# Kernel tuning notes

Hardware: AMD Instinct MI355X
Metric: run time of the kernel (lower is better)

The kernel has to match this reference:

```python
import jax, jax.numpy as jnp
import numpy as np

BN_EPS = 1e-5

def _conv3x3(x, w):
    # x: [N,C,H,W], w: [O,I,3,3], stride 1, padding 1, no bias
    return jax.lax.conv_general_dilated(
        x, w, window_strides=(1, 1), padding=((1, 1), (1, 1)),
        dimension_numbers=("NCHW", "OIHW", "NCHW"))

def _batchnorm(x, gamma, beta):
    # training-mode BN: batch statistics over (N,H,W)
    mean = jnp.mean(x, axis=(0, 2, 3), keepdims=True)
    var = jnp.mean(jnp.square(x - mean), axis=(0, 2, 3), keepdims=True)
    inv = jax.lax.rsqrt(var + BN_EPS)
    g = gamma.reshape(1, -1, 1, 1)
    b = beta.reshape(1, -1, 1, 1)
    return (x - mean) * inv * g + b

def setup_inputs() -> dict:
    key = jax.random.key(0)
    ks = jax.random.split(key, 3)
    x = jax.random.normal(ks[0], (32, 64, 128, 128), dtype=jnp.float32)
    # He-style scaled 3x3 conv kernels
    w1 = jax.random.normal(ks[1], (64, 64, 3, 3), dtype=jnp.float32) * (2.0 / (64 * 9)) ** 0.5
    w2 = jax.random.normal(ks[2], (64, 64, 3, 3), dtype=jnp.float32) * (2.0 / (64 * 9)) ** 0.5
    return {
        "x": x, "w1": w1, "w2": w2,
        "bn1_gamma": jnp.ones((64,), jnp.float32),
        "bn1_beta": jnp.zeros((64,), jnp.float32),
        "bn2_gamma": jnp.ones((64,), jnp.float32),
        "bn2_beta": jnp.zeros((64,), jnp.float32),
    }

def reference(x, w1, w2, bn1_gamma, bn1_beta, bn2_gamma, bn2_beta):
    out = _batchnorm(_conv3x3(x, w1), bn1_gamma, bn1_beta)
    out = _conv3x3(out, w2)
    out = out + x  # option 'A', stride=1, planes[2]==planes[0] -> identity shortcut
    return _batchnorm(out, bn2_gamma, bn2_beta)
```

## Files before the change

kernel.cpp:

```cpp
#include <hip/hip_runtime.h>
#include <hip/hip_bf16.h>

#define NB 32
#define CH 64
#define HH 128
#define WW 128
#define HW (HH*WW)
#define CHW (CH*HW)
#define NCHW (NB*CHW)
#define CNT_PER_CH ((float)(NB*HW))
#define ROWS 4

typedef __attribute__((ext_vector_type(8)))  short short8;
typedef __attribute__((ext_vector_type(16))) float f32x16;

__device__ __forceinline__ unsigned short f2bf(float f) {
  unsigned u = __builtin_bit_cast(unsigned, f);
  u += 0x7fffu + ((u >> 16) & 1u);
  return (unsigned short)(u >> 16);
}

__device__ __forceinline__ void gld_lds16(const void* g, void* s) {
  __builtin_amdgcn_global_load_lds(
      (const __attribute__((address_space(1))) unsigned int*)g,
      (__attribute__((address_space(3))) unsigned int*)s, 16, 0, 0);
}

__global__ __launch_bounds__(256) void t1_pack(const float* __restrict__ x,
                                               unsigned short* __restrict__ xb) {
  __shared__ __align__(16) unsigned short tmp[CH * WW];
  const int bid = blockIdx.x;
  const int tid = threadIdx.x;
  const float* src = x + (size_t)(bid >> 7) * CHW + (size_t)(bid & 127) * WW;
  for (int i = tid; i < 2048; i += 256) {
    const int ci = i >> 5, wq = i & 31;
    const float4 v = *(const float4*)(src + (size_t)ci * HW + wq * 4);
    unsigned short* d = &tmp[ci * WW + wq * 4];
    d[0] = f2bf(v.x); d[1] = f2bf(v.y); d[2] = f2bf(v.z); d[3] = f2bf(v.w);
  }
  __syncthreads();
  unsigned short* dst = xb + (size_t)bid * 8192;
  for (int i = tid; i < 1024; i += 256) {
    const int cb = i >> 7, w = i & 127;
    const unsigned short* s = &tmp[cb * 8 * WW + w];
    uint4 o;
    o.x = (unsigned)s[0]      | ((unsigned)s[WW]     << 16);
    o.y = (unsigned)s[2*WW]   | ((unsigned)s[3*WW]   << 16);
    o.z = (unsigned)s[4*WW]   | ((unsigned)s[5*WW]   << 16);
    o.w = (unsigned)s[6*WW]   | ((unsigned)s[7*WW]   << 16);
    *(uint4*)(dst + ((size_t)cb * WW + w) * 8) = o;
  }
}

__global__ __launch_bounds__(256) void pack_w(const float* __restrict__ w,
                                              const float* __restrict__ s1,
                                              const float* __restrict__ b1,
                                              unsigned short* __restrict__ wpk,
                                              float* __restrict__ tabs) {
  const int tid = threadIdx.x;
  for (int idx = tid; idx < 36864; idx += 256) {
    const int f = idx >> 9, l = (idx >> 3) & 63, r = idx & 7;
    const int m = f & 1, kq = (f >> 1) & 3, t = f >> 3;
    const int co = (l & 31) + 32 * m;
    const int ci = kq * 16 + (l >> 5) * 8 + r;
    float v = w[co * 576 + ci * 9 + t];
    if (s1) v *= s1[ci];
    wpk[idx] = f2bf(v);
  }
  if (tabs != nullptr && tid < 64) {
    const int co = tid;
    float tb[9];
    for (int t = 0; t < 9; ++t) {
      float a = 0.f;
      for (int ci = 0; ci < 64; ++ci) a += w[co * 576 + ci * 9 + t] * b1[ci];
      tb[t] = a;
    }
    tabs[0*64+co] = tb[0]+tb[1]+tb[2]+tb[3]+tb[4]+tb[5]+tb[6]+tb[7]+tb[8];
    tabs[1*64+co] = tb[0]+tb[1]+tb[2];
    tabs[2*64+co] = tb[6]+tb[7]+tb[8];
    tabs[3*64+co] = tb[0]+tb[3]+tb[6];
    tabs[4*64+co] = tb[2]+tb[5]+tb[8];
    tabs[5*64+co] = tb[0]; tabs[6*64+co] = tb[2];
    tabs[7*64+co] = tb[6]; tabs[8*64+co] = tb[8];
  }
}

template <bool IS2>
__global__ __launch_bounds__(256, 2)
void conv_mfma(const unsigned short* __restrict__ inb,
               const unsigned short* __restrict__ wpack,
               const float* __restrict__ tabs,
               const float* __restrict__ resid,
               unsigned short* __restrict__ outb,
               float* __restrict__ outf,
               float* __restrict__ psum, float* __restrict__ psq) {
  extern __shared__ __align__(16) unsigned short A[];
  const int tid = threadIdx.x, bid = blockIdx.x;
  const int n = bid >> 5, h0 = (bid & 31) << 2;
  const int wv = tid >> 6, lane = tid & 63;
  const int half = lane >> 5, lp = lane & 31;
  const int m  = wv & 1;
  const int nb = (wv >> 1) << 1;

  auto stage = [&](int ir) {
    const int sl = (ir + 4) & 3;
#pragma unroll
    for (int t = 0; t < 4; ++t) {
      const int id = wv + 4 * t;
      const int cb = id >> 1, wh = id & 1;
      unsigned short* dst = &A[(((sl * 8 + cb) * 130) + 1 + wh * 64) * 8];
      if ((unsigned)ir < 128u) {
        const unsigned short* g = inb + ((((size_t)n * 128 + ir) * 8 + cb) << 10)
                                      + (size_t)(wh * 64 + lane) * 8;
        gld_lds16(g, dst);
      } else {
        *(uint4*)(dst + (size_t)lane * 8) = make_uint4(0, 0, 0, 0);
      }
    }
  };

  if (tid < 64) {
    const int sl = tid >> 4, cb = (tid >> 1) & 7, s = (tid & 1) ? 129 : 0;
    *(uint4*)&A[(((sl * 8 + cb) * 130) + s) * 8] = make_uint4(0, 0, 0, 0);
  }

  short8 wr[36];
#pragma unroll
  for (int i = 0; i < 36; ++i) {
    const int f = ((i >> 2) << 3) + ((i & 3) << 1) + m;
    wr[i] = *(const short8*)(wpack + (size_t)f * 512 + (size_t)lane * 8);
  }

  stage(h0 - 1); stage(h0); stage(h0 + 1);

  for (int k = 0; k < ROWS; ++k) {
    const int r = h0 + k;
    __syncthreads();

    float rv[2][16];
    if (IS2) {
#pragma unroll
      for (int nt = 0; nt < 2; ++nt) {
        const int px = (nb + nt) * 32 + lp;
#pragma unroll
        for (int rr = 0; rr < 16; ++rr) {
          const int co = (rr & 3) + ((rr >> 2) << 3) + 4 * half + 32 * m;
          rv[nt][rr] = resid[(((size_t)n * 64 + co) * 128 + r) * 128 + px];
        }
      }
    }

    if (k < ROWS - 1) stage(r + 2);

    const int sl_m1 = (r + 3) & 3, sl_0 = (r + 4) & 3, sl_p1 = (r + 5) & 3;
    const int slot[3] = {sl_m1, sl_0, sl_p1};
    f32x16 acc0 = {}; f32x16 acc1 = {};
#pragma unroll
    for (int kh = 0; kh < 3; ++kh) {
      const int sb = slot[kh] * 8;
#pragma unroll
      for (int kw = 0; kw < 3; ++kw) {
#pragma unroll
        for (int kq = 0; kq < 4; ++kq) {
          const short8 wf = wr[(kh * 3 + kw) * 4 + kq];
          const int cb = kq * 2 + half;
          const unsigned short* base = &A[((sb + cb) * 130) * 8];
          const short8 b0 = *(const short8*)&base[(nb * 32 + lp + kw) * 8];
          const short8 b1 = *(const short8*)&base[((nb + 1) * 32 + lp + kw) * 8];
          acc0 = __builtin_amdgcn_mfma_f32_32x32x16_bf16(wf, b0, acc0, 0, 0, 0);
          acc1 = __builtin_amdgcn_mfma_f32_32x32x16_bf16(wf, b1, acc1, 0, 0, 0);
        }
      }
    }

    if (!IS2) {
      unsigned short* dst = outb + (((size_t)n * 128 + r) << 13);
#pragma unroll
      for (int nt = 0; nt < 2; ++nt) {
        const f32x16& a = nt ? acc1 : acc0;
        const int px = (nb + nt) * 32 + lp;
#pragma unroll
        for (int rq = 0; rq < 4; ++rq) {
          uint2 pk;
          pk.x = (unsigned)f2bf(a[rq*4+0]) | ((unsigned)f2bf(a[rq*4+1]) << 16);
          pk.y = (unsigned)f2bf(a[rq*4+2]) | ((unsigned)f2bf(a[rq*4+3]) << 16);
          *(uint2*)(dst + (((size_t)(rq + 4*m)) << 10) + (size_t)px * 8 + half * 4) = pk;
        }
      }
    } else {
      const bool bh0 = (r == 0), bh1 = (r == 127);
#pragma unroll
      for (int nt = 0; nt < 2; ++nt) {
        f32x16& a = nt ? acc1 : acc0;
        const int px = (nb + nt) * 32 + lp;
        const bool bw0 = (px == 0), bw1 = (px == 127);
#pragma unroll
        for (int rr = 0; rr < 16; ++rr) {
          const int co = (rr & 3) + ((rr >> 2) << 3) + 4 * half + 32 * m;
          float tb = tabs[co];
          if (bh0) tb -= tabs[64 + co];
          if (bh1) tb -= tabs[128 + co];
          if (bw0) tb -= tabs[192 + co];
          if (bw1) tb -= tabs[256 + co];
          if (bh0 && bw0) tb += tabs[320 + co];
          if (bh0 && bw1) tb += tabs[384 + co];
          if (bh1 && bw0) tb += tabs[448 + co];
          if (bh1 && bw1) tb += tabs[512 + co];
          const float v = a[rr] + tb + rv[nt][rr];
          outf[(((size_t)n * 64 + co) * 128 + r) * 128 + px] = v;
          a[rr] = v;
        }
      }
    }

#pragma unroll
    for (int rr = 0; rr < 16; ++rr) {
      float s = acc0[rr] + acc1[rr];
      float q = acc0[rr] * acc0[rr] + acc1[rr] * acc1[rr];
      s += __shfl_xor(s, 1);  q += __shfl_xor(q, 1);
      s += __shfl_xor(s, 2);  q += __shfl_xor(q, 2);
      s += __shfl_xor(s, 4);  q += __shfl_xor(q, 4);
      s += __shfl_xor(s, 8);  q += __shfl_xor(q, 8);
      s += __shfl_xor(s, 16); q += __shfl_xor(q, 16);
      if (lp == 0) {
        const int co = (rr & 3) + ((rr >> 2) << 3) + 4 * half + 32 * m;
        atomicAdd(&psum[(bid & 63) * 64 + co], s);
        atomicAdd(&psq [(bid & 63) * 64 + co], q);
      }
    }
  }
}

__global__ void finalize_bn(const float* __restrict__ psum, const float* __restrict__ psq,
                            const float* __restrict__ gamma, const float* __restrict__ beta,
                            float* __restrict__ scale, float* __restrict__ bias) {
  const int c = threadIdx.x;
  if (c < 64) {
    float s = 0.f, q = 0.f;
    for (int i = 0; i < 64; ++i) { s += psum[i * 64 + c]; q += psq[i * 64 + c]; }
    const float mean = s * (1.0f / CNT_PER_CH);
    const float var  = q * (1.0f / CNT_PER_CH) - mean * mean;
    const float inv  = rsqrtf(var + 1e-5f);
    const float sc   = inv * gamma[c];
    scale[c] = sc;
    bias[c]  = beta[c] - mean * sc;
  }
}

__global__ __launch_bounds__(256)
void apply_bn_k(float* __restrict__ out,
                const float* __restrict__ scale, const float* __restrict__ bias) {
  __shared__ float sc[CH], bs[CH];
  if (threadIdx.x < CH) { sc[threadIdx.x] = scale[threadIdx.x]; bs[threadIdx.x] = bias[threadIdx.x]; }
  __syncthreads();
  const size_t total4 = NCHW / 4;
  for (size_t i = (size_t)blockIdx.x * blockDim.x + threadIdx.x; i < total4;
       i += (size_t)gridDim.x * blockDim.x) {
    float4 v = reinterpret_cast<float4*>(out)[i];
    const int c = (int)(((i * 4) >> 14) & 63);
    const float s = sc[c], b = bs[c];
    v.x = fmaf(v.x, s, b);
    v.y = fmaf(v.y, s, b);
    v.z = fmaf(v.z, s, b);
    v.w = fmaf(v.w, s, b);
    reinterpret_cast<float4*>(out)[i] = v;
  }
}

extern "C" void kernel_launch(void* const* d_in, const int* in_sizes, int n_in,
                              void* d_out, int out_size, void* d_ws, size_t ws_size,
                              hipStream_t stream) {
  const float* x  = (const float*)d_in[0];
  const float* w1 = (const float*)d_in[1];
  const float* w2 = (const float*)d_in[2];
  const float* g1 = (const float*)d_in[3];
  const float* b1 = (const float*)d_in[4];
  const float* g2 = (const float*)d_in[5];
  const float* b2 = (const float*)d_in[6];
  float* out = (float*)d_out;
  char* ws = (char*)d_ws;

  unsigned short* XB  = (unsigned short*)ws;
  unsigned short* Y1B = (unsigned short*)(ws + 67108864);
  unsigned short* W2P = (unsigned short*)ws;
  float* TABS = (float*)(ws + 73728);
  float* SC1  = (float*)(ws + 76032);
  float* BS1  = (float*)(ws + 76288);
  float* SC2  = (float*)(ws + 76544);
  float* BS2  = (float*)(ws + 76800);
  float* P2S  = (float*)(ws + 77056);
  float* P2Q  = (float*)(ws + 93440);
  char* ob = (char*)d_out;
  unsigned short* W1P = (unsigned short*)ob;
  float* P1S = (float*)(ob + 73728);
  float* P1Q = (float*)(ob + 90112);

  const size_t conv_lds = 4 * 8 * 130 * 8 * sizeof(unsigned short);

  hipMemsetAsync(ob + 73728, 0, 32768, stream);
  pack_w<<<1, 256, 0, stream>>>(w1, nullptr, nullptr, W1P, nullptr);
  t1_pack<<<4096, 256, 0, stream>>>(x, XB);
  conv_mfma<false><<<1024, 256, conv_lds, stream>>>(XB, W1P, nullptr, nullptr,
                                                    Y1B, nullptr, P1S, P1Q);
  finalize_bn<<<1, 64, 0, stream>>>(P1S, P1Q, g1, b1, SC1, BS1);
  hipMemsetAsync(ws + 77056, 0, 32768, stream);
  pack_w<<<1, 256, 0, stream>>>(w2, SC1, BS1, W2P, TABS);
  conv_mfma<true><<<1024, 256, conv_lds, stream>>>(Y1B, W2P, TABS, x,
                                                   nullptr, out, P2S, P2Q);
  finalize_bn<<<1, 64, 0, stream>>>(P2S, P2Q, g2, b2, SC2, BS2);
  apply_bn_k<<<2048, 256, 0, stream>>>(out, SC2, BS2);
}
```

Measured before the change: 559.1 us.

## Replace per-row atomic BN stat reduction with per-block partials, drop memsets

Batch-norm sums and squared sums are now accumulated in registers across all rows of a block. They are reduced through wave shuffles and LDS, and each block writes one plain partial per channel, replacing the atomicAdds issued every row. The finalize kernel now uses 256 threads to reduce 1024 block partials, so both hipMemsetAsync calls are removed. This cuts atomic traffic and launches in exchange for a larger partial buffer and a longer serial reduction in finalize.

Measured after the change: 555.0 us. About the same (-0.7%).

```diff
diff --git a/kernel.cpp b/kernel.cpp
--- a/kernel.cpp
+++ b/kernel.cpp
@@ -10,6 +10,7 @@
 #define NCHW (NB*CHW)
 #define CNT_PER_CH ((float)(NB*HW))
 #define ROWS 4
+#define NBLK 1024
 
 typedef __attribute__((ext_vector_type(8)))  short short8;
 typedef __attribute__((ext_vector_type(16))) float f32x16;
@@ -93,7 +94,7 @@
                const float* __restrict__ resid,
                unsigned short* __restrict__ outb,
                float* __restrict__ outf,
-               float* __restrict__ psum, float* __restrict__ psq) {
+               float* __restrict__ pblk_s, float* __restrict__ pblk_q) {
   extern __shared__ __align__(16) unsigned short A[];
   const int tid = threadIdx.x, bid = blockIdx.x;
   const int n = bid >> 5, h0 = (bid & 31) << 2;
@@ -130,6 +131,10 @@
     const int f = ((i >> 2) << 3) + ((i & 3) << 1) + m;
     wr[i] = *(const short8*)(wpack + (size_t)f * 512 + (size_t)lane * 8);
   }
+
+  float ss[16], qq[16];
+#pragma unroll
+  for (int i = 0; i < 16; ++i) { ss[i] = 0.f; qq[i] = 0.f; }
 
   stage(h0 - 1); stage(h0); stage(h0 + 1);
 
@@ -215,29 +220,54 @@
 
 #pragma unroll
     for (int rr = 0; rr < 16; ++rr) {
-      float s = acc0[rr] + acc1[rr];
-      float q = acc0[rr] * acc0[rr] + acc1[rr] * acc1[rr];
-      s += __shfl_xor(s, 1);  q += __shfl_xor(q, 1);
-      s += __shfl_xor(s, 2);  q += __shfl_xor(q, 2);
-      s += __shfl_xor(s, 4);  q += __shfl_xor(q, 4);
-      s += __shfl_xor(s, 8);  q += __shfl_xor(q, 8);
-      s += __shfl_xor(s, 16); q += __shfl_xor(q, 16);
-      if (lp == 0) {
-        const int co = (rr & 3) + ((rr >> 2) << 3) + 4 * half + 32 * m;
-        atomicAdd(&psum[(bid & 63) * 64 + co], s);
-        atomicAdd(&psq [(bid & 63) * 64 + co], q);
-      }
-    }
-  }
-}
-
-__global__ void finalize_bn(const float* __restrict__ psum, const float* __restrict__ psq,
-                            const float* __restrict__ gamma, const float* __restrict__ beta,
-                            float* __restrict__ scale, float* __restrict__ bias) {
-  const int c = threadIdx.x;
-  if (c < 64) {
-    float s = 0.f, q = 0.f;
-    for (int i = 0; i < 64; ++i) { s += psum[i * 64 + c]; q += psq[i * 64 + c]; }
+      ss[rr] += acc0[rr] + acc1[rr];
+      qq[rr] += acc0[rr] * acc0[rr] + acc1[rr] * acc1[rr];
+    }
+  }
+
+  __syncthreads();
+  float* SLs = (float*)A;
+  float* SLq = SLs + 128;
+  const int p = wv >> 1;
+#pragma unroll
+  for (int rr = 0; rr < 16; ++rr) {
+    float s = ss[rr], q = qq[rr];
+    s += __shfl_xor(s, 1);  q += __shfl_xor(q, 1);
+    s += __shfl_xor(s, 2);  q += __shfl_xor(q, 2);
+    s += __shfl_xor(s, 4);  q += __shfl_xor(q, 4);
+    s += __shfl_xor(s, 8);  q += __shfl_xor(q, 8);
+    s += __shfl_xor(s, 16); q += __shfl_xor(q, 16);
+    if (lp == 0) {
+      const int co = (rr & 3) + ((rr >> 2) << 3) + 4 * half + 32 * m;
+      SLs[p * 64 + co] = s;
+      SLq[p * 64 + co] = q;
+    }
+  }
+  __syncthreads();
+  if (tid < 64) {
+    pblk_s[(size_t)bid * 64 + tid] = SLs[tid] + SLs[64 + tid];
+  } else if (tid < 128) {
+    const int co = tid - 64;
+    pblk_q[(size_t)bid * 64 + co] = SLq[co] + SLq[64 + co];
+  }
+}
+
+__global__ __launch_bounds__(256)
+void finalize_bn(const float* __restrict__ pblk_s, const float* __restrict__ pblk_q,
+                 const float* __restrict__ gamma, const float* __restrict__ beta,
+                 float* __restrict__ scale, float* __restrict__ bias) {
+  __shared__ float ls[4][64], lq[4][64];
+  const int c = threadIdx.x & 63, seg = threadIdx.x >> 6;
+  float s = 0.f, q = 0.f;
+  for (int i = seg * (NBLK / 4); i < (seg + 1) * (NBLK / 4); ++i) {
+    s += pblk_s[(size_t)i * 64 + c];
+    q += pblk_q[(size_t)i * 64 + c];
+  }
+  ls[seg][c] = s; lq[seg][c] = q;
+  __syncthreads();
+  if (threadIdx.x < 64) {
+    s = ls[0][c] + ls[1][c] + ls[2][c] + ls[3][c];
+    q = lq[0][c] + lq[1][c] + lq[2][c] + lq[3][c];
     const float mean = s * (1.0f / CNT_PER_CH);
     const float var  = q * (1.0f / CNT_PER_CH) - mean * mean;
     const float inv  = rsqrtf(var + 1e-5f);
@@ -288,25 +318,23 @@
   float* BS1  = (float*)(ws + 76288);
   float* SC2  = (float*)(ws + 76544);
   float* BS2  = (float*)(ws + 76800);
-  float* P2S  = (float*)(ws + 77056);
-  float* P2Q  = (float*)(ws + 93440);
+  float* P2S  = (float*)(ws + 131072);
+  float* P2Q  = (float*)(ws + 131072 + 262144);
   char* ob = (char*)d_out;
   unsigned short* W1P = (unsigned short*)ob;
   float* P1S = (float*)(ob + 73728);
-  float* P1Q = (float*)(ob + 90112);
+  float* P1Q = (float*)(ob + 73728 + 262144);
 
   const size_t conv_lds = 4 * 8 * 130 * 8 * sizeof(unsigned short);
 
-  hipMemsetAsync(ob + 73728, 0, 32768, stream);
   pack_w<<<1, 256, 0, stream>>>(w1, nullptr, nullptr, W1P, nullptr);
   t1_pack<<<4096, 256, 0, stream>>>(x, XB);
-  conv_mfma<false><<<1024, 256, conv_lds, stream>>>(XB, W1P, nullptr, nullptr,
+  conv_mfma<false><<<NBLK, 256, conv_lds, stream>>>(XB, W1P, nullptr, nullptr,
                                                     Y1B, nullptr, P1S, P1Q);
-  finalize_bn<<<1, 64, 0, stream>>>(P1S, P1Q, g1, b1, SC1, BS1);
-  hipMemsetAsync(ws + 77056, 0, 32768, stream);
+  finalize_bn<<<1, 256, 0, stream>>>(P1S, P1Q, g1, b1, SC1, BS1);
   pack_w<<<1, 256, 0, stream>>>(w2, SC1, BS1, W2P, TABS);
-  conv_mfma<true><<<1024, 256, conv_lds, stream>>>(Y1B, W2P, TABS, x,
+  conv_mfma<true><<<NBLK, 256, conv_lds, stream>>>(Y1B, W2P, TABS, x,
                                                    nullptr, out, P2S, P2Q);
-  finalize_bn<<<1, 64, 0, stream>>>(P2S, P2Q, g2, b2, SC2, BS2);
+  finalize_bn<<<1, 256, 0, stream>>>(P2S, P2Q, g2, b2, SC2, BS2);
   apply_bn_k<<<2048, 256, 0, stream>>>(out, SC2, BS2);
 }
```
